# Optimization experiments

Measured on AMD Instinct MI355X. Metric: run time of the kernel, lower is better.

The kernel has to match this reference:

```python
import jax, jax.numpy as jnp
import numpy as np

N, E = 100000, 1600000
IN_DIM, HID_DIM, OUT_DIM = 128, 64, 32


def setup_inputs() -> dict:
    key = jax.random.key(0)
    k1, k2, k3, k4 = jax.random.split(key, 4)
    x = jax.random.normal(k1, (N, IN_DIM), dtype=jnp.float32)
    edge_index = jax.random.randint(k2, (2, E), 0, N, dtype=jnp.int64)
    # GCNConv weights (glorot) and zero biases, matching PyG defaults
    s1 = float(np.sqrt(6.0 / (IN_DIM + HID_DIM)))
    s2 = float(np.sqrt(6.0 / (HID_DIM + OUT_DIM)))
    W1 = jax.random.uniform(k3, (IN_DIM, HID_DIM), jnp.float32, -s1, s1)
    W2 = jax.random.uniform(k4, (HID_DIM, OUT_DIM), jnp.float32, -s2, s2)
    b1 = jnp.zeros((HID_DIM,), jnp.float32)
    b2 = jnp.zeros((OUT_DIM,), jnp.float32)
    return {"x": x, "W1": W1, "b1": b1, "W2": W2, "b2": b2, "edge_index": edge_index}


def _gcn_conv(x, W, b, row, col, n):
    # x: [N, Fin] -> [N, Fout].  row/col already include self-loops.
    xw = x @ W  # [N, Fout]
    deg = jax.ops.segment_sum(jnp.ones_like(col, dtype=xw.dtype), col, num_segments=n)
    dinv = jnp.where(deg > 0, jax.lax.rsqrt(deg), jnp.zeros_like(deg))
    norm = dinv[row] * dinv[col]  # [E+N]
    out = jax.ops.segment_sum(norm[:, None] * xw[row], col, num_segments=n)
    return out + b


def reference(x, W1, b1, W2, b2, edge_index):
    n = x.shape[0]
    loops = jnp.arange(n, dtype=edge_index.dtype)
    row = jnp.concatenate([edge_index[0], loops])
    col = jnp.concatenate([edge_index[1], loops])
    h = jax.nn.relu(_gcn_conv(x, W1, b1, row, col, n))
    # F.dropout with training=False is the identity (eval-mode reference)
    out = jax.nn.relu(_gcn_conv(h, W2, b2, row, col, n))
    return out
```

## Files before the change

### kernel.cpp

```cpp
#include <hip/hip_runtime.h>

#define IN_DIM  128
#define HID_DIM 64
#define OUT_DIM 32
#define BPN   256
#define CHUNK 4096
#define STRIDE1 8192
#define STRIDE2 (STRIDE1 + 8 * BPN)

typedef __attribute__((ext_vector_type(8))) short bf16x8;
typedef __attribute__((ext_vector_type(4))) float f32x4;

__device__ __forceinline__ unsigned pack_bf16(float a, float b) {
  unsigned ua = __float_as_uint(a), ub = __float_as_uint(b);
  ua += 0x7FFFu + ((ua >> 16) & 1u);
  ub += 0x7FFFu + ((ub >> 16) & 1u);
  return (ua >> 16) | (ub & 0xFFFF0000u);
}
__device__ __forceinline__ float bf_lo(unsigned v) { return __uint_as_float(v << 16); }
__device__ __forceinline__ float bf_hi(unsigned v) { return __uint_as_float(v & 0xFFFF0000u); }

__device__ __forceinline__ int load_idx(const void* p, long long i, int is64) {
  return is64 ? (int)((const long long*)p)[i] : ((const int*)p)[i];
}

__device__ __forceinline__ int block_detect(const void* eidx, long long E,
                                            long long N, int* sflag) {
  bool ok = true;
  long long cap = E < 64 ? E : 64;
  if (threadIdx.x < cap)
    ok = ((const unsigned long long*)eidx)[threadIdx.x] < (unsigned long long)N;
  unsigned long long ball = __ballot(ok);
  if (threadIdx.x == 0) *sflag = (ball == ~0ULL) ? 1 : 0;
  __syncthreads();
  return *sflag;
}

__global__ __launch_bounds__(512) void k_zero(int* __restrict__ binCursor) {
  binCursor[threadIdx.x] = 0;
}

__global__ __launch_bounds__(512) void k_prep(const float* __restrict__ W1,
                                              unsigned short* __restrict__ w1t,
                                              unsigned* __restrict__ xw1b,
                                              unsigned* __restrict__ xw2b, int N) {
  int t = threadIdx.x;
  if (t < HID_DIM / 2) xw1b[(size_t)N * (HID_DIM / 2) + t] = 0;
  else if (t < HID_DIM / 2 + OUT_DIM / 2)
    xw2b[(size_t)N * (OUT_DIM / 2) + (t - HID_DIM / 2)] = 0;
  for (int i = t; i < HID_DIM * IN_DIM; i += 512) {
    int j = i >> 7, k = i & 127;
    w1t[i] = (unsigned short)(pack_bf16(W1[k * HID_DIM + j], 0.f) & 0xFFFFu);
  }
}

__global__ __launch_bounds__(256) void k_p2(const void* eidx, long long E,
                                            int* __restrict__ binCursor,
                                            unsigned* __restrict__ entry1,
                                            long long N, int nbin) {
  __shared__ int hist[512];
  __shared__ int basel[512];
  __shared__ int sflag;
  for (int i = threadIdx.x; i < nbin; i += 256) hist[i] = 0;
  int f = block_detect(eidx, E, N, &sflag);
  long long b0 = (long long)blockIdx.x * CHUNK;
#pragma unroll
  for (int i = 0; i < CHUNK / 256; ++i) {
    long long e = b0 + i * 256 + threadIdx.x;
    if (e < E) atomicAdd(&hist[load_idx(eidx, E + e, f) >> 8], 1);
  }
  __syncthreads();
  for (int i = threadIdx.x; i < nbin; i += 256) {
    int h = hist[i];
    basel[i] = h ? atomicAdd(&binCursor[i], h) : 0;
  }
  __syncthreads();
  for (int i = threadIdx.x; i < nbin; i += 256) hist[i] = 0;
  __syncthreads();
#pragma unroll
  for (int i = 0; i < CHUNK / 256; ++i) {
    long long e = b0 + i * 256 + threadIdx.x;
    if (e < E) {
      int r = load_idx(eidx, e, f);
      int c = load_idx(eidx, E + e, f);
      int bin = c >> 8;
      int rk = basel[bin] + atomicAdd(&hist[bin], 1);
      if (rk < STRIDE1)
        entry1[(size_t)bin * STRIDE1 + rk] = ((unsigned)(c & 255) << 17) | (unsigned)r;
    }
  }
}

__global__ __launch_bounds__(256) void k_p3(const unsigned* __restrict__ entry1,
                                            const int* __restrict__ binCursor,
                                            int* __restrict__ entry2,
                                            int* __restrict__ base,
                                            int* __restrict__ cnt,
                                            float* __restrict__ dinv, int N) {
  __shared__ int hist[BPN];
  __shared__ int off[BPN];
  __shared__ int s[BPN];
  int t = threadIdx.x;
  int b = blockIdx.x;
  int lo = b * STRIDE1;
  int ec = binCursor[b]; if (ec > STRIDE1) ec = STRIDE1;
  int hi = lo + ec;
  int pBB = b * STRIDE2;
  int n0 = b * BPN;
  hist[t] = 0;
  __syncthreads();
  for (int i = lo + t; i < hi; i += 256)
    atomicAdd(&hist[entry1[i] >> 17], 1);
  __syncthreads();
  int own  = hist[t];
  int own8 = (own + 7) & ~7;
  s[t] = own8; __syncthreads();
  for (int o = 1; o < 256; o <<= 1) {
    int v = (t >= o) ? s[t - o] : 0;
    __syncthreads();
    s[t] += v;
    __syncthreads();
  }
  int node = n0 + t;
  int ex = pBB + (s[t] - own8);
  if (node < N) {
    base[node] = ex;
    cnt[node]  = own;
    dinv[node] = rsqrtf((float)own + 1.0f);
    for (int q = own; q < own8; ++q) entry2[ex + q] = N;
  }
  off[t] = ex;
  __syncthreads();
  for (int i = lo + t; i < hi; i += 256) {
    unsigned v = entry1[i];
    int pos = atomicAdd(&off[v >> 17], 1);
    entry2[pos] = (int)(v & 0x1FFFFu);
  }
}

__global__ __launch_bounds__(256) void k_gemm1(const float* __restrict__ x,
                                               const unsigned short* __restrict__ w1t,
                                               const float* __restrict__ dinv,
                                               unsigned* __restrict__ xw1b, int N) {
  __shared__ unsigned short xs[64 * IN_DIM];
  __shared__ unsigned short wt[64 * IN_DIM];
  const int rbase = blockIdx.x * 64;

  {
    const float4* xg = (const float4*)x;
#pragma unroll
    for (int j = 0; j < 8; ++j) {
      int fIdx = threadIdx.x + 256 * j;
      int r = fIdx >> 5, c4 = fIdx & 31;
      int rr = rbase + r; if (rr >= N) rr = N - 1;
      float4 v = xg[(size_t)rr * 32 + c4];
      uint2 pv = make_uint2(pack_bf16(v.x, v.y), pack_bf16(v.z, v.w));
      int chunk = (c4 >> 1) ^ (r & 7);
      *(uint2*)((char*)xs + r * 256 + chunk * 16 + (c4 & 1) * 8) = pv;
    }
  }
  {
    const uint2* wg = (const uint2*)w1t;
#pragma unroll
    for (int j = 0; j < 8; ++j) {
      int fIdx = threadIdx.x + 256 * j;
      int r = fIdx >> 5, q = fIdx & 31;
      uint2 v = wg[fIdx];
      int chunk = (q >> 1) ^ (r & 7);
      *(uint2*)((char*)wt + r * 256 + chunk * 16 + (q & 1) * 8) = v;
    }
  }
  __syncthreads();

  const int wv = threadIdx.x >> 6;
  const int l  = threadIdx.x & 63;
  const int lo16 = l & 15;
  const int hi4  = l >> 4;

  bf16x8 a[4];
#pragma unroll
  for (int ks = 0; ks < 4; ++ks) {
    int row = wv * 16 + lo16;
    int chunk = (ks * 4 + hi4) ^ (row & 7);
    a[ks] = *(const bf16x8*)((const char*)xs + row * 256 + chunk * 16);
  }

  f32x4 acc[4];
#pragma unroll
  for (int ct = 0; ct < 4; ++ct) {
    f32x4 c = {0.f, 0.f, 0.f, 0.f};
#pragma unroll
    for (int ks = 0; ks < 4; ++ks) {
      int col = ct * 16 + lo16;
      int chunk = (ks * 4 + hi4) ^ (col & 7);
      bf16x8 b = *(const bf16x8*)((const char*)wt + col * 256 + chunk * 16);
      c = __builtin_amdgcn_mfma_f32_16x16x32_bf16(a[ks], b, c, 0, 0, 0);
    }
    acc[ct] = c;
  }

  float dvr[4];
#pragma unroll
  for (int i = 0; i < 4; ++i) {
    int row = rbase + wv * 16 + hi4 * 4 + i;
    dvr[i] = (row < N) ? dinv[row] : 0.f;
  }
#pragma unroll
  for (int ct = 0; ct < 4; ++ct) {
#pragma unroll
    for (int i = 0; i < 4; ++i) {
      float v = dvr[i] * acc[ct][i];
      float vp = __shfl_xor(v, 1);
      int row = rbase + wv * 16 + hi4 * 4 + i;
      if ((l & 1) == 0 && row < N) {
        int j = ct * 16 + lo16;
        xw1b[(size_t)row * (HID_DIM / 2) + (j >> 1)] = pack_bf16(v, vp);
      }
    }
  }
}

__global__ __launch_bounds__(256) void k_gather1(const int* __restrict__ entry,
                                                 const int* __restrict__ base,
                                                 const int* __restrict__ cnt,
                                                 const float* __restrict__ dinv,
                                                 const uint2* __restrict__ xw1b2,
                                                 const float* __restrict__ b1,
                                                 const float* __restrict__ W2,
                                                 unsigned* __restrict__ xw2b, int N) {
  __shared__ float w2s[HID_DIM * OUT_DIM];
  __shared__ float hs[16][68];
  __shared__ float dvs[16];
  for (int i = threadIdx.x; i < HID_DIM * OUT_DIM; i += 256) w2s[i] = W2[i];
  __syncthreads();

  const int wv   = threadIdx.x >> 6;
  const int ln   = threadIdx.x & 63;
  const int slot = wv * 4 + (ln >> 4);
  const int lane = ln & 15;
  const int node = blockIdx.x * 16 + slot;

  if (node < N) {
    int st = base[node];
    int it = (cnt[node] + 7) >> 3;
    float ax[4], ay[4], az[4], aw[4];
#pragma unroll
    for (int q = 0; q < 4; ++q) { ax[q] = ay[q] = az[q] = aw[q] = 0.f; }
    for (int i = 0; i < it; ++i) {
      int4 ea = *(const int4*)(entry + st + 8 * i);
      int4 eb = *(const int4*)(entry + st + 8 * i + 4);
      uint2 v0 = xw1b2[(size_t)ea.x * 16 + lane];
      uint2 v1 = xw1b2[(size_t)ea.y * 16 + lane];
      uint2 v2 = xw1b2[(size_t)ea.z * 16 + lane];
      uint2 v3 = xw1b2[(size_t)ea.w * 16 + lane];
      uint2 v4 = xw1b2[(size_t)eb.x * 16 + lane];
      uint2 v5 = xw1b2[(size_t)eb.y * 16 + lane];
      uint2 v6 = xw1b2[(size_t)eb.z * 16 + lane];
      uint2 v7 = xw1b2[(size_t)eb.w * 16 + lane];
      ax[0] += bf_lo(v0.x) + bf_lo(v4.x); ay[0] += bf_hi(v0.x) + bf_hi(v4.x);
      az[0] += bf_lo(v0.y) + bf_lo(v4.y); aw[0] += bf_hi(v0.y) + bf_hi(v4.y);
      ax[1] += bf_lo(v1.x) + bf_lo(v5.x); ay[1] += bf_hi(v1.x) + bf_hi(v5.x);
      az[1] += bf_lo(v1.y) + bf_lo(v5.y); aw[1] += bf_hi(v1.y) + bf_hi(v5.y);
      ax[2] += bf_lo(v2.x) + bf_lo(v6.x); ay[2] += bf_hi(v2.x) + bf_hi(v6.x);
      az[2] += bf_lo(v2.y) + bf_lo(v6.y); aw[2] += bf_hi(v2.y) + bf_hi(v6.y);
      ax[3] += bf_lo(v3.x) + bf_lo(v7.x); ay[3] += bf_hi(v3.x) + bf_hi(v7.x);
      az[3] += bf_lo(v3.y) + bf_lo(v7.y); aw[3] += bf_hi(v3.y) + bf_hi(v7.y);
    }
    uint2 vs = xw1b2[(size_t)node * 16 + lane];
    float dv = dinv[node];
    float4 bb = *(const float4*)(b1 + 4 * lane);
    float h0 = dv * ((ax[0] + ax[1]) + (ax[2] + ax[3]) + bf_lo(vs.x)) + bb.x;
    float h1 = dv * ((ay[0] + ay[1]) + (ay[2] + ay[3]) + bf_hi(vs.x)) + bb.y;
    float h2 = dv * ((az[0] + az[1]) + (az[2] + az[3]) + bf_lo(vs.y)) + bb.z;
    float h3 = dv * ((aw[0] + aw[1]) + (aw[2] + aw[3]) + bf_hi(vs.y)) + bb.w;
    float4 hv;
    hv.x = h0 > 0.f ? h0 : 0.f;
    hv.y = h1 > 0.f ? h1 : 0.f;
    hv.z = h2 > 0.f ? h2 : 0.f;
    hv.w = h3 > 0.f ? h3 : 0.f;
    *(float4*)(&hs[slot][4 * lane]) = hv;
    if (lane == 0) dvs[slot] = dv;
  }
  __builtin_amdgcn_wave_barrier();

  if (node < N) {
    float acc0 = 0.f, acc1 = 0.f;
#pragma unroll
    for (int jj = 0; jj < HID_DIM; ++jj) {
      float hv = hs[slot][jj];
      float2 w = *(const float2*)(w2s + jj * OUT_DIM + 2 * lane);
      acc0 += hv * w.x;
      acc1 += hv * w.y;
    }
    float dv = dvs[slot];
    xw2b[(size_t)node * (OUT_DIM / 2) + lane] = pack_bf16(dv * acc0, dv * acc1);
  }
}

__global__ __launch_bounds__(256) void k_gather2(const int* __restrict__ entry,
                                                 const int* __restrict__ base,
                                                 const int* __restrict__ cnt,
                                                 const float* __restrict__ dinv,
                                                 const uint2* __restrict__ xw2b2,
                                                 const float* __restrict__ b2,
                                                 float* __restrict__ out, int N) {
  const int nl   = threadIdx.x >> 3;
  const int lane = threadIdx.x & 7;
  const int node = blockIdx.x * 32 + nl;
  if (node >= N) return;
  int st = base[node];
  int it = (cnt[node] + 7) >> 3;
  float ax[4], ay[4], az[4], aw[4];
#pragma unroll
  for (int q = 0; q < 4; ++q) { ax[q] = ay[q] = az[q] = aw[q] = 0.f; }
  for (int i = 0; i < it; ++i) {
    int4 ea = *(const int4*)(entry + st + 8 * i);
    int4 eb = *(const int4*)(entry + st + 8 * i + 4);
    uint2 v0 = xw2b2[(size_t)ea.x * 8 + lane];
    uint2 v1 = xw2b2[(size_t)ea.y * 8 + lane];
    uint2 v2 = xw2b2[(size_t)ea.z * 8 + lane];
    uint2 v3 = xw2b2[(size_t)ea.w * 8 + lane];
    uint2 v4 = xw2b2[(size_t)eb.x * 8 + lane];
    uint2 v5 = xw2b2[(size_t)eb.y * 8 + lane];
    uint2 v6 = xw2b2[(size_t)eb.z * 8 + lane];
    uint2 v7 = xw2b2[(size_t)eb.w * 8 + lane];
    ax[0] += bf_lo(v0.x) + bf_lo(v4.x); ay[0] += bf_hi(v0.x) + bf_hi(v4.x);
    az[0] += bf_lo(v0.y) + bf_lo(v4.y); aw[0] += bf_hi(v0.y) + bf_hi(v4.y);
    ax[1] += bf_lo(v1.x) + bf_lo(v5.x); ay[1] += bf_hi(v1.x) + bf_hi(v5.x);
    az[1] += bf_lo(v1.y) + bf_lo(v5.y); aw[1] += bf_hi(v1.y) + bf_hi(v5.y);
    ax[2] += bf_lo(v2.x) + bf_lo(v6.x); ay[2] += bf_hi(v2.x) + bf_hi(v6.x);
    az[2] += bf_lo(v2.y) + bf_lo(v6.y); aw[2] += bf_hi(v2.y) + bf_hi(v6.y);
    ax[3] += bf_lo(v3.x) + bf_lo(v7.x); ay[3] += bf_hi(v3.x) + bf_hi(v7.x);
    az[3] += bf_lo(v3.y) + bf_lo(v7.y); aw[3] += bf_hi(v3.y) + bf_hi(v7.y);
  }
  uint2 vs = xw2b2[(size_t)node * 8 + lane];
  float dv = dinv[node];
  float4 bb = *(const float4*)(b2 + 4 * lane);
  float v0 = dv * ((ax[0] + ax[1]) + (ax[2] + ax[3]) + bf_lo(vs.x)) + bb.x;
  float v1 = dv * ((ay[0] + ay[1]) + (ay[2] + ay[3]) + bf_hi(vs.x)) + bb.y;
  float v2 = dv * ((az[0] + az[1]) + (az[2] + az[3]) + bf_lo(vs.y)) + bb.z;
  float v3 = dv * ((aw[0] + aw[1]) + (aw[2] + aw[3]) + bf_hi(vs.y)) + bb.w;
  float4 res;
  res.x = v0 > 0.f ? v0 : 0.f;
  res.y = v1 > 0.f ? v1 : 0.f;
  res.z = v2 > 0.f ? v2 : 0.f;
  res.w = v3 > 0.f ? v3 : 0.f;
  *(float4*)(out + (size_t)node * OUT_DIM + 4 * lane) = res;
}

static inline size_t align256(size_t x) { return (x + 255) & ~(size_t)255; }

extern "C" void kernel_launch(void* const* d_in, const int* in_sizes, int n_in,
                              void* d_out, int out_size, void* d_ws, size_t ws_size,
                              hipStream_t stream) {
  const float* x   = (const float*)d_in[0];
  const float* W1  = (const float*)d_in[1];
  const float* b1  = (const float*)d_in[2];
  const float* W2  = (const float*)d_in[3];
  const float* b2  = (const float*)d_in[4];
  const void*  eidx = d_in[5];

  const int  N = in_sizes[0] / IN_DIM;
  const long long E = (long long)in_sizes[5] / 2;
  const int  nbin = (N + BPN - 1) / BPN;
  const int  np   = (int)((E + CHUNK - 1) / CHUNK);

  char* ws = (char*)d_ws;
  size_t off = 0;
  int*      cnt       = (int*)(ws + off);      off += align256((size_t)N * 4);
  float*    dinv      = (float*)(ws + off);    off += align256((size_t)N * 4);
  int*      base      = (int*)(ws + off);      off += align256((size_t)N * 4);
  int*      binCursor = (int*)(ws + off);      off += align256(512 * 4);
  unsigned short* w1t = (unsigned short*)(ws + off); off += align256((size_t)HID_DIM * IN_DIM * 2);
  unsigned* entry1    = (unsigned*)(ws + off); off += align256((size_t)nbin * STRIDE1 * 4);
  int*      entry2    = (int*)(ws + off);      off += align256((size_t)nbin * STRIDE2 * 4);
  unsigned* xw1b      = (unsigned*)(ws + off); off += align256((size_t)(N + 1) * (HID_DIM / 2) * 4);
  unsigned* xw2b      = (unsigned*)(ws + off); off += align256((size_t)(N + 1) * (OUT_DIM / 2) * 4);
  float*    outf      = (float*)d_out;

  k_zero<<<1, 512, 0, stream>>>(binCursor);
  k_prep<<<1, 512, 0, stream>>>(W1, w1t, xw1b, xw2b, N);

  k_p2<<<np, 256, 0, stream>>>(eidx, E, binCursor, entry1, (long long)N, nbin);
  k_p3<<<nbin, 256, 0, stream>>>(entry1, binCursor, entry2, base, cnt, dinv, N);

  k_gemm1<<<(N + 63) / 64, 256, 0, stream>>>(x, w1t, dinv, xw1b, N);

  k_gather1<<<(N + 15) / 16, 256, 0, stream>>>(entry2, base, cnt, dinv,
                                               (const uint2*)xw1b, b1, W2, xw2b, N);

  k_gather2<<<(N + 31) / 32, 256, 0, stream>>>(entry2, base, cnt, dinv,
                                               (const uint2*)xw2b, b2, outf, N);
}
```

Baseline: 128.3 us.

## Halve bucket size to 128 nodes and cache column indices in k_p2 registers

Shrinks the node bin from 256 to 128 (with half-size chunks and strides), doubling the number of bins and p3 blocks. Raises the p2 block size to 512 threads and holds the destination indices in registers, so the second pass does not reload them from global memory. The aim is more parallelism in the bucket-sort phase and less index traffic. In exchange, half the threads in k_p3 sit idle, more global bin-cursor atomics are issued, and the per-bin capacity of 4096 edges still drops entries on overflow.

```diff
diff --git a/kernel.cpp b/kernel.cpp
--- a/kernel.cpp
+++ b/kernel.cpp
@@ -3,9 +3,9 @@
 #define IN_DIM  128
 #define HID_DIM 64
 #define OUT_DIM 32
-#define BPN   256
-#define CHUNK 4096
-#define STRIDE1 8192
+#define BPN   128
+#define CHUNK 2048
+#define STRIDE1 4096
 #define STRIDE2 (STRIDE1 + 8 * BPN)
 
 typedef __attribute__((ext_vector_type(8))) short bf16x8;
@@ -38,6 +38,7 @@
 
 __global__ __launch_bounds__(512) void k_zero(int* __restrict__ binCursor) {
   binCursor[threadIdx.x] = 0;
+  binCursor[512 + threadIdx.x] = 0;
 }
 
 __global__ __launch_bounds__(512) void k_prep(const float* __restrict__ W1,
@@ -54,39 +55,44 @@
   }
 }
 
-__global__ __launch_bounds__(256) void k_p2(const void* eidx, long long E,
+__global__ __launch_bounds__(512) void k_p2(const void* eidx, long long E,
                                             int* __restrict__ binCursor,
                                             unsigned* __restrict__ entry1,
                                             long long N, int nbin) {
-  __shared__ int hist[512];
-  __shared__ int basel[512];
+  __shared__ int hist[1024];
+  __shared__ int basel[1024];
   __shared__ int sflag;
-  for (int i = threadIdx.x; i < nbin; i += 256) hist[i] = 0;
+  for (int i = threadIdx.x; i < nbin; i += 512) hist[i] = 0;
   int f = block_detect(eidx, E, N, &sflag);
   long long b0 = (long long)blockIdx.x * CHUNK;
-#pragma unroll
-  for (int i = 0; i < CHUNK / 256; ++i) {
-    long long e = b0 + i * 256 + threadIdx.x;
-    if (e < E) atomicAdd(&hist[load_idx(eidx, E + e, f) >> 8], 1);
-  }
-  __syncthreads();
-  for (int i = threadIdx.x; i < nbin; i += 256) {
+
+  int cv[CHUNK / 512];
+#pragma unroll
+  for (int i = 0; i < CHUNK / 512; ++i) {
+    long long e = b0 + i * 512 + threadIdx.x;
+    cv[i] = (e < E) ? load_idx(eidx, E + e, f) : -1;
+  }
+#pragma unroll
+  for (int i = 0; i < CHUNK / 512; ++i)
+    if (cv[i] >= 0) atomicAdd(&hist[cv[i] >> 7], 1);
+  __syncthreads();
+  for (int i = threadIdx.x; i < nbin; i += 512) {
     int h = hist[i];
     basel[i] = h ? atomicAdd(&binCursor[i], h) : 0;
   }
   __syncthreads();
-  for (int i = threadIdx.x; i < nbin; i += 256) hist[i] = 0;
-  __syncthreads();
-#pragma unroll
-  for (int i = 0; i < CHUNK / 256; ++i) {
-    long long e = b0 + i * 256 + threadIdx.x;
-    if (e < E) {
+  for (int i = threadIdx.x; i < nbin; i += 512) hist[i] = 0;
+  __syncthreads();
+#pragma unroll
+  for (int i = 0; i < CHUNK / 512; ++i) {
+    if (cv[i] >= 0) {
+      long long e = b0 + i * 512 + threadIdx.x;
       int r = load_idx(eidx, e, f);
-      int c = load_idx(eidx, E + e, f);
-      int bin = c >> 8;
+      int c = cv[i];
+      int bin = c >> 7;
       int rk = basel[bin] + atomicAdd(&hist[bin], 1);
       if (rk < STRIDE1)
-        entry1[(size_t)bin * STRIDE1 + rk] = ((unsigned)(c & 255) << 17) | (unsigned)r;
+        entry1[(size_t)bin * STRIDE1 + rk] = ((unsigned)(c & 127) << 17) | (unsigned)r;
     }
   }
 }
@@ -107,29 +113,35 @@
   int hi = lo + ec;
   int pBB = b * STRIDE2;
   int n0 = b * BPN;
-  hist[t] = 0;
+  if (t < BPN) hist[t] = 0;
   __syncthreads();
   for (int i = lo + t; i < hi; i += 256)
     atomicAdd(&hist[entry1[i] >> 17], 1);
   __syncthreads();
-  int own  = hist[t];
-  int own8 = (own + 7) & ~7;
-  s[t] = own8; __syncthreads();
-  for (int o = 1; o < 256; o <<= 1) {
-    int v = (t >= o) ? s[t - o] : 0;
+  int own = 0, own8 = 0;
+  if (t < BPN) {
+    own  = hist[t];
+    own8 = (own + 7) & ~7;
+    s[t] = own8;
+  }
+  __syncthreads();
+  for (int o = 1; o < BPN; o <<= 1) {
+    int v = (t < BPN && t >= o) ? s[t - o] : 0;
     __syncthreads();
-    s[t] += v;
+    if (t < BPN) s[t] += v;
     __syncthreads();
   }
   int node = n0 + t;
-  int ex = pBB + (s[t] - own8);
-  if (node < N) {
-    base[node] = ex;
-    cnt[node]  = own;
-    dinv[node] = rsqrtf((float)own + 1.0f);
-    for (int q = own; q < own8; ++q) entry2[ex + q] = N;
-  }
-  off[t] = ex;
+  if (t < BPN) {
+    int ex = pBB + (s[t] - own8);
+    if (node < N) {
+      base[node] = ex;
+      cnt[node]  = own;
+      dinv[node] = rsqrtf((float)own + 1.0f);
+      for (int q = own; q < own8; ++q) entry2[ex + q] = N;
+    }
+    off[t] = ex;
+  }
   __syncthreads();
   for (int i = lo + t; i < hi; i += 256) {
     unsigned v = entry1[i];
@@ -370,7 +382,7 @@
   int*      cnt       = (int*)(ws + off);      off += align256((size_t)N * 4);
   float*    dinv      = (float*)(ws + off);    off += align256((size_t)N * 4);
   int*      base      = (int*)(ws + off);      off += align256((size_t)N * 4);
-  int*      binCursor = (int*)(ws + off);      off += align256(512 * 4);
+  int*      binCursor = (int*)(ws + off);      off += align256(1024 * 4);
   unsigned short* w1t = (unsigned short*)(ws + off); off += align256((size_t)HID_DIM * IN_DIM * 2);
   unsigned* entry1    = (unsigned*)(ws + off); off += align256((size_t)nbin * STRIDE1 * 4);
   int*      entry2    = (int*)(ws + off);      off += align256((size_t)nbin * STRIDE2 * 4);
@@ -381,7 +393,7 @@
   k_zero<<<1, 512, 0, stream>>>(binCursor);
   k_prep<<<1, 512, 0, stream>>>(W1, w1t, xw1b, xw2b, N);
 
-  k_p2<<<np, 256, 0, stream>>>(eidx, E, binCursor, entry1, (long long)N, nbin);
+  k_p2<<<np, 512, 0, stream>>>(eidx, E, binCursor, entry1, (long long)N, nbin);
   k_p3<<<nbin, 256, 0, stream>>>(entry1, binCursor, entry2, base, cnt, dinv, N);
 
   k_gemm1<<<(N + 63) / 64, 256, 0, stream>>>(x, w1t, dinv, xw1b, N);
```

New measurement: 132.2 us. 3.0% more time.

## Replace global bin-cursor atomics with per-block fixed-capacity cells in edge bucketing

Applied to the files above, without the earlier changes.

Edge binning now writes each block's edges into a fixed-capacity cell per (bin, block) and records per-cell counts, so the global atomic cursor, its zeroing kernel and the separate counting pass are gone. Bins grow to 512 nodes and chunks to 8192 edges with 512-thread blocks, and the scatter kernel walks the cells using the recorded counts. Indices are loaded once into registers instead of twice. Cells hold at most 96 edges, so a skewed degree distribution would silently drop edges, and the scatter kernel must scan every padded slot.

```diff
diff --git a/kernel.cpp b/kernel.cpp
--- a/kernel.cpp
+++ b/kernel.cpp
@@ -3,10 +3,10 @@
 #define IN_DIM  128
 #define HID_DIM 64
 #define OUT_DIM 32
-#define BPN   256
-#define CHUNK 4096
-#define STRIDE1 8192
-#define STRIDE2 (STRIDE1 + 8 * BPN)
+#define BPN   512
+#define CHUNK 8192
+#define CAP   96
+#define STRIDE2 16384
 
 typedef __attribute__((ext_vector_type(8))) short bf16x8;
 typedef __attribute__((ext_vector_type(4))) float f32x4;
@@ -34,10 +34,6 @@
   if (threadIdx.x == 0) *sflag = (ball == ~0ULL) ? 1 : 0;
   __syncthreads();
   return *sflag;
-}
-
-__global__ __launch_bounds__(512) void k_zero(int* __restrict__ binCursor) {
-  binCursor[threadIdx.x] = 0;
 }
 
 __global__ __launch_bounds__(512) void k_prep(const float* __restrict__ W1,
@@ -54,75 +50,75 @@
   }
 }
 
-__global__ __launch_bounds__(256) void k_p2(const void* eidx, long long E,
-                                            int* __restrict__ binCursor,
+__global__ __launch_bounds__(512) void k_p2(const void* eidx, long long E,
                                             unsigned* __restrict__ entry1,
-                                            long long N, int nbin) {
-  __shared__ int hist[512];
-  __shared__ int basel[512];
+                                            int* __restrict__ cellCnt,
+                                            long long N, int nbin, int np) {
+  __shared__ int hist[256];
   __shared__ int sflag;
-  for (int i = threadIdx.x; i < nbin; i += 256) hist[i] = 0;
+  for (int i = threadIdx.x; i < nbin; i += 512) hist[i] = 0;
   int f = block_detect(eidx, E, N, &sflag);
-  long long b0 = (long long)blockIdx.x * CHUNK;
-#pragma unroll
-  for (int i = 0; i < CHUNK / 256; ++i) {
-    long long e = b0 + i * 256 + threadIdx.x;
-    if (e < E) atomicAdd(&hist[load_idx(eidx, E + e, f) >> 8], 1);
-  }
-  __syncthreads();
-  for (int i = threadIdx.x; i < nbin; i += 256) {
-    int h = hist[i];
-    basel[i] = h ? atomicAdd(&binCursor[i], h) : 0;
-  }
-  __syncthreads();
-  for (int i = threadIdx.x; i < nbin; i += 256) hist[i] = 0;
-  __syncthreads();
-#pragma unroll
-  for (int i = 0; i < CHUNK / 256; ++i) {
-    long long e = b0 + i * 256 + threadIdx.x;
-    if (e < E) {
-      int r = load_idx(eidx, e, f);
-      int c = load_idx(eidx, E + e, f);
-      int bin = c >> 8;
-      int rk = basel[bin] + atomicAdd(&hist[bin], 1);
-      if (rk < STRIDE1)
-        entry1[(size_t)bin * STRIDE1 + rk] = ((unsigned)(c & 255) << 17) | (unsigned)r;
-    }
-  }
-}
-
-__global__ __launch_bounds__(256) void k_p3(const unsigned* __restrict__ entry1,
-                                            const int* __restrict__ binCursor,
+  const int blk = blockIdx.x;
+  long long b0 = (long long)blk * CHUNK;
+
+  int cv[CHUNK / 512], rv[CHUNK / 512];
+#pragma unroll
+  for (int i = 0; i < CHUNK / 512; ++i) {
+    long long e = b0 + i * 512 + threadIdx.x;
+    cv[i] = (e < E) ? load_idx(eidx, E + e, f) : -1;
+    rv[i] = (e < E) ? load_idx(eidx, e, f) : 0;
+  }
+#pragma unroll
+  for (int i = 0; i < CHUNK / 512; ++i) {
+    if (cv[i] >= 0) {
+      int c = cv[i];
+      int bin = c >> 9;
+      int rk = atomicAdd(&hist[bin], 1);
+      if (rk < CAP)
+        entry1[((size_t)bin * np + blk) * CAP + rk] =
+            ((unsigned)(c & (BPN - 1)) << 17) | (unsigned)rv[i];
+    }
+  }
+  __syncthreads();
+  for (int i = threadIdx.x; i < nbin; i += 512)
+    cellCnt[(size_t)blk * nbin + i] = hist[i] < CAP ? hist[i] : CAP;
+}
+
+__global__ __launch_bounds__(512) void k_p3(const unsigned* __restrict__ entry1,
+                                            const int* __restrict__ cellCnt,
                                             int* __restrict__ entry2,
                                             int* __restrict__ base,
                                             int* __restrict__ cnt,
-                                            float* __restrict__ dinv, int N) {
+                                            float* __restrict__ dinv,
+                                            int N, int nbin, int np) {
+  __shared__ int cc[256];
   __shared__ int hist[BPN];
   __shared__ int off[BPN];
   __shared__ int s[BPN];
-  int t = threadIdx.x;
-  int b = blockIdx.x;
-  int lo = b * STRIDE1;
-  int ec = binCursor[b]; if (ec > STRIDE1) ec = STRIDE1;
-  int hi = lo + ec;
-  int pBB = b * STRIDE2;
-  int n0 = b * BPN;
+  const int t = threadIdx.x;
+  const int b = blockIdx.x;
+  if (t < np) cc[t] = cellCnt[(size_t)t * nbin + b];
   hist[t] = 0;
   __syncthreads();
-  for (int i = lo + t; i < hi; i += 256)
-    atomicAdd(&hist[entry1[i] >> 17], 1);
+
+  const unsigned* e1 = entry1 + (size_t)b * np * CAP;
+  const int nslots = np * CAP;
+  for (int sIdx = t; sIdx < nslots; sIdx += 512) {
+    int blk = sIdx / CAP, sl = sIdx - blk * CAP;
+    if (sl < cc[blk]) atomicAdd(&hist[e1[sIdx] >> 17], 1);
+  }
   __syncthreads();
   int own  = hist[t];
   int own8 = (own + 7) & ~7;
   s[t] = own8; __syncthreads();
-  for (int o = 1; o < 256; o <<= 1) {
+  for (int o = 1; o < BPN; o <<= 1) {
     int v = (t >= o) ? s[t - o] : 0;
     __syncthreads();
     s[t] += v;
     __syncthreads();
   }
-  int node = n0 + t;
-  int ex = pBB + (s[t] - own8);
+  int node = b * BPN + t;
+  int ex = b * STRIDE2 + (s[t] - own8);
   if (node < N) {
     base[node] = ex;
     cnt[node]  = own;
@@ -131,10 +127,13 @@
   }
   off[t] = ex;
   __syncthreads();
-  for (int i = lo + t; i < hi; i += 256) {
-    unsigned v = entry1[i];
-    int pos = atomicAdd(&off[v >> 17], 1);
-    entry2[pos] = (int)(v & 0x1FFFFu);
+  for (int sIdx = t; sIdx < nslots; sIdx += 512) {
+    int blk = sIdx / CAP, sl = sIdx - blk * CAP;
+    if (sl < cc[blk]) {
+      unsigned v = e1[sIdx];
+      int pos = atomicAdd(&off[v >> 17], 1);
+      entry2[pos] = (int)(v & 0x1FFFFu);
+    }
   }
 }
 
@@ -370,19 +369,18 @@
   int*      cnt       = (int*)(ws + off);      off += align256((size_t)N * 4);
   float*    dinv      = (float*)(ws + off);    off += align256((size_t)N * 4);
   int*      base      = (int*)(ws + off);      off += align256((size_t)N * 4);
-  int*      binCursor = (int*)(ws + off);      off += align256(512 * 4);
+  int*      cellCnt   = (int*)(ws + off);      off += align256((size_t)np * nbin * 4);
   unsigned short* w1t = (unsigned short*)(ws + off); off += align256((size_t)HID_DIM * IN_DIM * 2);
-  unsigned* entry1    = (unsigned*)(ws + off); off += align256((size_t)nbin * STRIDE1 * 4);
+  unsigned* entry1    = (unsigned*)(ws + off); off += align256((size_t)nbin * np * CAP * 4);
   int*      entry2    = (int*)(ws + off);      off += align256((size_t)nbin * STRIDE2 * 4);
   unsigned* xw1b      = (unsigned*)(ws + off); off += align256((size_t)(N + 1) * (HID_DIM / 2) * 4);
   unsigned* xw2b      = (unsigned*)(ws + off); off += align256((size_t)(N + 1) * (OUT_DIM / 2) * 4);
   float*    outf      = (float*)d_out;
 
-  k_zero<<<1, 512, 0, stream>>>(binCursor);
   k_prep<<<1, 512, 0, stream>>>(W1, w1t, xw1b, xw2b, N);
 
-  k_p2<<<np, 256, 0, stream>>>(eidx, E, binCursor, entry1, (long long)N, nbin);
-  k_p3<<<nbin, 256, 0, stream>>>(entry1, binCursor, entry2, base, cnt, dinv, N);
+  k_p2<<<np, 512, 0, stream>>>(eidx, E, entry1, cellCnt, (long long)N, nbin, np);
+  k_p3<<<nbin, 512, 0, stream>>>(entry1, cellCnt, entry2, base, cnt, dinv, N, nbin, np);
 
   k_gemm1<<<(N + 63) / 64, 256, 0, stream>>>(x, w1t, dinv, xw1b, N);
 
```

After: 122.5 us. 4.6% less time.
